# Optimization experiments

Hardware: AMD Instinct MI355X
Metric: run time of the kernel (lower is better)

## Reference

```python
import jax, jax.numpy as jnp
import numpy as np


def setup_inputs() -> dict:
    key = jax.random.key(0)
    k1, k2, k3 = jax.random.split(key, 3)
    B, F, H, W = 16, 16, 256, 256
    inp = jax.random.normal(k1, (B, F, H, W), dtype=jnp.float32)
    target = jax.random.normal(k2, (B, F, H, W), dtype=jnp.float32)
    masks = jax.random.randint(k3, (B, F, H, W), 0, 2).astype(jnp.bool_)
    hull = jnp.zeros((1,), dtype=jnp.int32)  # unused by the module's forward
    return {"input": inp, "target": target, "masks": masks, "hull": hull}


def _masked_mean_per_feature(diff, w):
    # diff: [B,F,H,W]; w: float mask broadcastable to diff. Returns [F] masked means
    # with 0.0 where the mask is empty (matching the torch `if len(diff) > 0` guard).
    s = jnp.sum(diff * w, axis=(0, 2, 3))                               # [F]
    c = jnp.sum(jnp.broadcast_to(w, diff.shape), axis=(0, 2, 3))        # [F]
    return jnp.where(c > 0, s / jnp.maximum(c, 1.0), 0.0)


def reference(input, target, masks, hull):
    diff = jnp.abs(input - target)                                      # [B,F,H,W]
    m = masks.astype(diff.dtype)                                        # feature masks
    m_not = 1.0 - m                                                     # background
    m_all = jnp.any(masks, axis=1, keepdims=True).astype(diff.dtype)    # [B,1,H,W]

    loss_features = jnp.mean(_masked_mean_per_feature(diff, m))
    loss_background = jnp.mean(_masked_mean_per_feature(diff, m_not))
    loss_all_features = jnp.mean(_masked_mean_per_feature(diff, m_all))

    return (loss_features + loss_all_features + loss_background) / 3.0
```

## Files before the change

### kernel.cpp

```cpp
#include <hip/hip_runtime.h>
#include <hip/hip_bf16.h>

constexpr int B = 16, F = 16, H = 256, W = 256;
constexpr int HW = H * W;
constexpr int SPATIAL = B * HW;
constexpr int NBLOCKS = 2048;
constexpr int NTHREADS = 512;
constexpr int NVALS = 65;
constexpr int PLANE4 = HW / 4;
constexpr int BSTRIDE4 = F * PLANE4;
constexpr int FQ = 4;

__global__ __launch_bounds__(NTHREADS, 6) void heatloss_main(
        const float4* __restrict__ inp, const float4* __restrict__ tgt,
        const unsigned int* __restrict__ msk, float* __restrict__ partials) {
    const int tid  = threadIdx.x;
    const int wave = tid >> 6;
    const int lane = tid & 63;
    const int l16  = lane & 15;
    const int q    = lane >> 4;
    const int g    = (blockIdx.x * 8 + wave) * 16 + l16;
    const int b    = g >> 14;
    const int hw4  = g & (PLANE4 - 1);
    const int base = b * BSTRIDE4 + hw4 + q * (FQ * PLANE4);

    unsigned int m[FQ];
    #pragma unroll
    for (int j = 0; j < FQ; j++) m[j] = msk[base + j * PLANE4];
    float4 av[FQ], tv[FQ];
    #pragma unroll
    for (int j = 0; j < FQ; j++) av[j] = inp[base + j * PLANE4];
    #pragma unroll
    for (int j = 0; j < FQ; j++) tv[j] = tgt[base + j * PLANE4];

    unsigned int anyu = m[0] | m[1] | m[2] | m[3];
    anyu |= __shfl_xor(anyu, 16, 64);
    anyu |= __shfl_xor(anyu, 32, 64);
    const float af0 = (anyu & 0x000000FFu) ? 1.f : 0.f;
    const float af1 = (anyu & 0x0000FF00u) ? 1.f : 0.f;
    const float af2 = (anyu & 0x00FF0000u) ? 1.f : 0.f;
    const float af3 = (anyu & 0xFF000000u) ? 1.f : 0.f;
    const float call = (q == 0) ? (af0 + af1) + (af2 + af3) : 0.f;

    float s[FQ], c[FQ], dtot[FQ], sall[FQ];
    #pragma unroll
    for (int j = 0; j < FQ; j++) {
        const float4 a = av[j];
        const float4 t = tv[j];
        const float d0 = fabsf(a.x - t.x);
        const float d1 = fabsf(a.y - t.y);
        const float d2 = fabsf(a.z - t.z);
        const float d3 = fabsf(a.w - t.w);
        const unsigned int mm = m[j];
        const float m0 = (float)( mm        & 0xFFu);
        const float m1 = (float)((mm >> 8)  & 0xFFu);
        const float m2 = (float)((mm >> 16) & 0xFFu);
        const float m3 = (float)( mm >> 24);
        dtot[j] = (d0 + d1) + (d2 + d3);
        s[j]    = m0 * d0 + m1 * d1 + m2 * d2 + m3 * d3;
        c[j]    = (m0 + m1) + (m2 + m3);
        sall[j] = af0 * d0 + af1 * d1 + af2 * d2 + af3 * d3;
    }

    __shared__ float red[NTHREADS / 64][NVALS];
    const int fbase = q * FQ;
    #pragma unroll
    for (int j = 0; j < FQ; j++) {
        float xs = s[j], xc = c[j], xd = dtot[j], xa = sall[j];
        #pragma unroll
        for (int o = 8; o > 0; o >>= 1) {
            xs += __shfl_down(xs, o, 16);
            xc += __shfl_down(xc, o, 16);
            xd += __shfl_down(xd, o, 16);
            xa += __shfl_down(xa, o, 16);
        }
        if (l16 == 0) {
            red[wave][ 0 + fbase + j] = xs;
            red[wave][16 + fbase + j] = xc;
            red[wave][32 + fbase + j] = xd;
            red[wave][48 + fbase + j] = xa;
        }
    }
    float xcall = call;
    #pragma unroll
    for (int o = 8; o > 0; o >>= 1) xcall += __shfl_down(xcall, o, 16);
    if (lane == 0) red[wave][64] = xcall;
    __syncthreads();
    if (tid < NVALS) {
        float t = 0.f;
        #pragma unroll
        for (int w2 = 0; w2 < NTHREADS / 64; w2++) t += red[w2][tid];
        partials[tid * NBLOCKS + blockIdx.x] = t;
    }
}

__global__ __launch_bounds__(256) void heatloss_reduce(
        const float* __restrict__ partials, float* __restrict__ vals) {
    const int v = blockIdx.x;
    const int t = threadIdx.x;
    const float* p = partials + v * NBLOCKS;
    float x = 0.f;
    #pragma unroll
    for (int k = 0; k < NBLOCKS / 256; k++) x += p[t + k * 256];
    #pragma unroll
    for (int o = 32; o > 0; o >>= 1) x += __shfl_down(x, o, 64);
    __shared__ float red[4];
    if ((t & 63) == 0) red[t >> 6] = x;
    __syncthreads();
    if (t == 0) vals[v] = (red[0] + red[1]) + (red[2] + red[3]);
}

__global__ __launch_bounds__(128) void heatloss_combine(
        const float* __restrict__ vals_in, float* __restrict__ out) {
    __shared__ float vals[NVALS];
    const int t = threadIdx.x;
    if (t < NVALS) vals[t] = vals_in[t];
    __syncthreads();
    if (t == 0) {
        const float Nf = (float)SPATIAL;
        const float call = vals[64];
        float lf = 0.f, lbg = 0.f, lall = 0.f;
        #pragma unroll
        for (int f = 0; f < F; f++) {
            const float sf = vals[f], cf = vals[16 + f];
            const float dt = vals[32 + f], sa = vals[48 + f];
            lf += (cf > 0.f) ? sf / cf : 0.f;
            const float sbg = dt - sf, cbg = Nf - cf;
            lbg += (cbg > 0.f) ? sbg / cbg : 0.f;
            lall += (call > 0.f) ? sa / call : 0.f;
        }
        out[0] = (lf / 16.f + lbg / 16.f + lall / 16.f) / 3.f;
    }
}

extern "C" void kernel_launch(void* const* d_in, const int* in_sizes, int n_in,
                              void* d_out, int out_size, void* d_ws, size_t ws_size,
                              hipStream_t stream) {
    const float4*       inp = (const float4*)d_in[0];
    const float4*       tgt = (const float4*)d_in[1];
    const unsigned int* msk = (const unsigned int*)d_in[2];
    float* out      = (float*)d_out;
    float* partials = (float*)d_ws;
    float* vals     = partials + NVALS * NBLOCKS;

    heatloss_main<<<NBLOCKS, NTHREADS, 0, stream>>>(inp, tgt, msk, partials);
    heatloss_reduce<<<NVALS, 256, 0, stream>>>(partials, vals);
    heatloss_combine<<<1, 128, 0, stream>>>(vals, out);
}
```

Before: 185.6 us.

## Fuse reduction kernels via last-block atomic counter with grid-stride double-buffered loads

Merges the three kernels into one. Blocks drop from 2048 to 512, and each thread walks a grid-stride loop with register double-buffering of the next iteration's loads. Because the all-features mask is feature-independent, its sum collapses into one scalar, cutting the per-block values from 65 to 50. The last block to finish, detected through an atomic counter, does the final reduction and combine. This removes two extra launches in exchange for a memset and a serialized tail reduction in a single block.

Result: slower. 213.1 us (+14.9%).

```diff
diff --git a/kernel.cpp b/kernel.cpp
--- a/kernel.cpp
+++ b/kernel.cpp
@@ -1,135 +1,167 @@
 #include <hip/hip_runtime.h>
-#include <hip/hip_bf16.h>
 
 constexpr int B = 16, F = 16, H = 256, W = 256;
 constexpr int HW = H * W;
 constexpr int SPATIAL = B * HW;
-constexpr int NBLOCKS = 2048;
-constexpr int NTHREADS = 512;
-constexpr int NVALS = 65;
 constexpr int PLANE4 = HW / 4;
 constexpr int BSTRIDE4 = F * PLANE4;
 constexpr int FQ = 4;
 
-__global__ __launch_bounds__(NTHREADS, 6) void heatloss_main(
+constexpr int NBLK = 512;
+constexpr int NTHREADS = 512;
+constexpr int NWAVES = NTHREADS / 64;
+constexpr int TOTG = B * PLANE4;
+constexpr int SLOTS = NBLK * NWAVES * 16;
+constexpr int G = TOTG / SLOTS;
+static_assert(TOTG % SLOTS == 0, "grid-stride must divide evenly");
+
+constexpr int NVALS = 50;
+
+__global__ __launch_bounds__(NTHREADS, 4) void heatloss_fused(
         const float4* __restrict__ inp, const float4* __restrict__ tgt,
-        const unsigned int* __restrict__ msk, float* __restrict__ partials) {
+        const unsigned int* __restrict__ msk, float* __restrict__ partials,
+        int* __restrict__ counter, float* __restrict__ out) {
     const int tid  = threadIdx.x;
     const int wave = tid >> 6;
     const int lane = tid & 63;
     const int l16  = lane & 15;
     const int q    = lane >> 4;
-    const int g    = (blockIdx.x * 8 + wave) * 16 + l16;
-    const int b    = g >> 14;
-    const int hw4  = g & (PLANE4 - 1);
-    const int base = b * BSTRIDE4 + hw4 + q * (FQ * PLANE4);
+    const int slot0 = (blockIdx.x * NWAVES + wave) * 16 + l16;
+    const int qoff  = q * (FQ * PLANE4);
 
-    unsigned int m[FQ];
-    #pragma unroll
-    for (int j = 0; j < FQ; j++) m[j] = msk[base + j * PLANE4];
-    float4 av[FQ], tv[FQ];
-    #pragma unroll
-    for (int j = 0; j < FQ; j++) av[j] = inp[base + j * PLANE4];
-    #pragma unroll
-    for (int j = 0; j < FQ; j++) tv[j] = tgt[base + j * PLANE4];
+    float s[FQ]  = {0.f, 0.f, 0.f, 0.f};
+    float c[FQ]  = {0.f, 0.f, 0.f, 0.f};
+    float dt[FQ] = {0.f, 0.f, 0.f, 0.f};
+    float sall = 0.f, call = 0.f;
 
-    unsigned int anyu = m[0] | m[1] | m[2] | m[3];
-    anyu |= __shfl_xor(anyu, 16, 64);
-    anyu |= __shfl_xor(anyu, 32, 64);
-    const float af0 = (anyu & 0x000000FFu) ? 1.f : 0.f;
-    const float af1 = (anyu & 0x0000FF00u) ? 1.f : 0.f;
-    const float af2 = (anyu & 0x00FF0000u) ? 1.f : 0.f;
-    const float af3 = (anyu & 0xFF000000u) ? 1.f : 0.f;
-    const float call = (q == 0) ? (af0 + af1) + (af2 + af3) : 0.f;
+    unsigned int mb[2][FQ];
+    float4 ab[2][FQ], tb[2][FQ];
 
-    float s[FQ], c[FQ], dtot[FQ], sall[FQ];
-    #pragma unroll
-    for (int j = 0; j < FQ; j++) {
-        const float4 a = av[j];
-        const float4 t = tv[j];
-        const float d0 = fabsf(a.x - t.x);
-        const float d1 = fabsf(a.y - t.y);
-        const float d2 = fabsf(a.z - t.z);
-        const float d3 = fabsf(a.w - t.w);
-        const unsigned int mm = m[j];
-        const float m0 = (float)( mm        & 0xFFu);
-        const float m1 = (float)((mm >> 8)  & 0xFFu);
-        const float m2 = (float)((mm >> 16) & 0xFFu);
-        const float m3 = (float)( mm >> 24);
-        dtot[j] = (d0 + d1) + (d2 + d3);
-        s[j]    = m0 * d0 + m1 * d1 + m2 * d2 + m3 * d3;
-        c[j]    = (m0 + m1) + (m2 + m3);
-        sall[j] = af0 * d0 + af1 * d1 + af2 * d2 + af3 * d3;
+    {
+        const int slot = slot0;
+        const int base = (slot >> 14) * BSTRIDE4 + (slot & (PLANE4 - 1)) + qoff;
+        #pragma unroll
+        for (int j = 0; j < FQ; j++) mb[0][j] = msk[base + j * PLANE4];
+        #pragma unroll
+        for (int j = 0; j < FQ; j++) ab[0][j] = inp[base + j * PLANE4];
+        #pragma unroll
+        for (int j = 0; j < FQ; j++) tb[0][j] = tgt[base + j * PLANE4];
     }
 
-    __shared__ float red[NTHREADS / 64][NVALS];
+    #pragma unroll
+    for (int it = 0; it < G; ++it) {
+        const int cur = it & 1, nxt = cur ^ 1;
+        if (it + 1 < G) {
+            const int slot = slot0 + (it + 1) * SLOTS;
+            const int base = (slot >> 14) * BSTRIDE4 + (slot & (PLANE4 - 1)) + qoff;
+            #pragma unroll
+            for (int j = 0; j < FQ; j++) mb[nxt][j] = msk[base + j * PLANE4];
+            #pragma unroll
+            for (int j = 0; j < FQ; j++) ab[nxt][j] = inp[base + j * PLANE4];
+            #pragma unroll
+            for (int j = 0; j < FQ; j++) tb[nxt][j] = tgt[base + j * PLANE4];
+        }
+
+        unsigned int anyu = mb[cur][0] | mb[cur][1] | mb[cur][2] | mb[cur][3];
+        anyu |= __shfl_xor(anyu, 16, 64);
+        anyu |= __shfl_xor(anyu, 32, 64);
+        const float af0 = (anyu & 0x000000FFu) ? 1.f : 0.f;
+        const float af1 = (anyu & 0x0000FF00u) ? 1.f : 0.f;
+        const float af2 = (anyu & 0x00FF0000u) ? 1.f : 0.f;
+        const float af3 = (anyu & 0xFF000000u) ? 1.f : 0.f;
+        if (q == 0) call += (af0 + af1) + (af2 + af3);
+
+        #pragma unroll
+        for (int j = 0; j < FQ; j++) {
+            const float4 a = ab[cur][j];
+            const float4 t = tb[cur][j];
+            const float d0 = fabsf(a.x - t.x);
+            const float d1 = fabsf(a.y - t.y);
+            const float d2 = fabsf(a.z - t.z);
+            const float d3 = fabsf(a.w - t.w);
+            const unsigned int mm = mb[cur][j];
+            const float m0 = (float)( mm        & 0xFFu);
+            const float m1 = (float)((mm >> 8)  & 0xFFu);
+            const float m2 = (float)((mm >> 16) & 0xFFu);
+            const float m3 = (float)( mm >> 24);
+            dt[j] += (d0 + d1) + (d2 + d3);
+            s[j]  += m0 * d0 + m1 * d1 + m2 * d2 + m3 * d3;
+            c[j]  += (m0 + m1) + (m2 + m3);
+            sall  += af0 * d0 + af1 * d1 + af2 * d2 + af3 * d3;
+        }
+    }
+
+    __shared__ float red[NWAVES][NVALS];
     const int fbase = q * FQ;
     #pragma unroll
     for (int j = 0; j < FQ; j++) {
-        float xs = s[j], xc = c[j], xd = dtot[j], xa = sall[j];
+        float xs = s[j], xc = c[j], xd = dt[j];
         #pragma unroll
         for (int o = 8; o > 0; o >>= 1) {
             xs += __shfl_down(xs, o, 16);
             xc += __shfl_down(xc, o, 16);
             xd += __shfl_down(xd, o, 16);
-            xa += __shfl_down(xa, o, 16);
         }
         if (l16 == 0) {
             red[wave][ 0 + fbase + j] = xs;
             red[wave][16 + fbase + j] = xc;
             red[wave][32 + fbase + j] = xd;
-            red[wave][48 + fbase + j] = xa;
         }
     }
-    float xcall = call;
+    float xa = sall, xcl = call;
     #pragma unroll
-    for (int o = 8; o > 0; o >>= 1) xcall += __shfl_down(xcall, o, 16);
-    if (lane == 0) red[wave][64] = xcall;
+    for (int o = 32; o > 0; o >>= 1) {
+        xa  += __shfl_down(xa,  o, 64);
+        xcl += __shfl_down(xcl, o, 64);
+    }
+    if (lane == 0) { red[wave][48] = xa; red[wave][49] = xcl; }
     __syncthreads();
+
     if (tid < NVALS) {
         float t = 0.f;
         #pragma unroll
-        for (int w2 = 0; w2 < NTHREADS / 64; w2++) t += red[w2][tid];
-        partials[tid * NBLOCKS + blockIdx.x] = t;
+        for (int w2 = 0; w2 < NWAVES; w2++) t += red[w2][tid];
+        __hip_atomic_store(&partials[tid * NBLK + blockIdx.x], t,
+                           __ATOMIC_RELAXED, __HIP_MEMORY_SCOPE_AGENT);
     }
-}
+    __syncthreads();
 
-__global__ __launch_bounds__(256) void heatloss_reduce(
-        const float* __restrict__ partials, float* __restrict__ vals) {
-    const int v = blockIdx.x;
-    const int t = threadIdx.x;
-    const float* p = partials + v * NBLOCKS;
-    float x = 0.f;
-    #pragma unroll
-    for (int k = 0; k < NBLOCKS / 256; k++) x += p[t + k * 256];
-    #pragma unroll
-    for (int o = 32; o > 0; o >>= 1) x += __shfl_down(x, o, 64);
-    __shared__ float red[4];
-    if ((t & 63) == 0) red[t >> 6] = x;
+    __shared__ int lastflag;
+    if (tid == 0) {
+        const int old = __hip_atomic_fetch_add(counter, 1, __ATOMIC_ACQ_REL,
+                                               __HIP_MEMORY_SCOPE_AGENT);
+        lastflag = (old == NBLK - 1) ? 1 : 0;
+    }
     __syncthreads();
-    if (t == 0) vals[v] = (red[0] + red[1]) + (red[2] + red[3]);
-}
 
-__global__ __launch_bounds__(128) void heatloss_combine(
-        const float* __restrict__ vals_in, float* __restrict__ out) {
-    __shared__ float vals[NVALS];
-    const int t = threadIdx.x;
-    if (t < NVALS) vals[t] = vals_in[t];
-    __syncthreads();
-    if (t == 0) {
-        const float Nf = (float)SPATIAL;
-        const float call = vals[64];
-        float lf = 0.f, lbg = 0.f, lall = 0.f;
-        #pragma unroll
-        for (int f = 0; f < F; f++) {
-            const float sf = vals[f], cf = vals[16 + f];
-            const float dt = vals[32 + f], sa = vals[48 + f];
-            lf += (cf > 0.f) ? sf / cf : 0.f;
-            const float sbg = dt - sf, cbg = Nf - cf;
-            lbg += (cbg > 0.f) ? sbg / cbg : 0.f;
-            lall += (call > 0.f) ? sa / call : 0.f;
+    if (lastflag) {
+        __shared__ float vals[NVALS];
+        for (int v = wave; v < NVALS; v += NWAVES) {
+            const float* p = partials + v * NBLK;
+            float x = 0.f;
+            #pragma unroll
+            for (int k = 0; k < NBLK / 64; k++)
+                x += __hip_atomic_load(p + lane + k * 64,
+                                       __ATOMIC_RELAXED, __HIP_MEMORY_SCOPE_AGENT);
+            #pragma unroll
+            for (int o = 32; o > 0; o >>= 1) x += __shfl_down(x, o, 64);
+            if (lane == 0) vals[v] = x;
         }
-        out[0] = (lf / 16.f + lbg / 16.f + lall / 16.f) / 3.f;
+        __syncthreads();
+        if (tid == 0) {
+            const float Nf = (float)SPATIAL;
+            float lf = 0.f, lbg = 0.f;
+            #pragma unroll
+            for (int f = 0; f < F; f++) {
+                const float sf = vals[f], cf = vals[16 + f], dtf = vals[32 + f];
+                lf += (cf > 0.f) ? sf / cf : 0.f;
+                const float sbg = dtf - sf, cbg = Nf - cf;
+                lbg += (cbg > 0.f) ? sbg / cbg : 0.f;
+            }
+            const float sa = vals[48], cl = vals[49];
+            const float lall = (cl > 0.f) ? sa / cl : 0.f;
+            out[0] = (lf / 16.f + lbg / 16.f + lall / 16.f) / 3.f;
+        }
     }
 }
 
@@ -141,9 +173,9 @@
     const unsigned int* msk = (const unsigned int*)d_in[2];
     float* out      = (float*)d_out;
     float* partials = (float*)d_ws;
-    float* vals     = partials + NVALS * NBLOCKS;
+    int*   counter  = (int*)(partials + NVALS * NBLK);
 
-    heatloss_main<<<NBLOCKS, NTHREADS, 0, stream>>>(inp, tgt, msk, partials);
-    heatloss_reduce<<<NVALS, 256, 0, stream>>>(partials, vals);
-    heatloss_combine<<<1, 128, 0, stream>>>(vals, out);
+    hipMemsetAsync(counter, 0, sizeof(int), stream);
+    heatloss_fused<<<NBLK, NTHREADS, 0, stream>>>(inp, tgt, msk, partials,
+                                                  counter, out);
 }
```
